# Optimization experiments

Hardware: AMD Instinct MI355X
Metric: run time of the kernel (lower is better)

Reference implementation:

```python
import jax, jax.numpy as jnp
import numpy as np

B, N, M, D = 8, 4096, 4096, 3


def setup_inputs() -> dict:
    key = jax.random.key(0)
    k1, k2 = jax.random.split(key)
    preds = jax.random.normal(k1, (B, M, D), dtype=jnp.float32)
    gts = jax.random.normal(k2, (B, N, D), dtype=jnp.float32)
    c = jnp.ones((1,), dtype=jnp.float32)
    return {"preds": preds, "gts": gts, "c": c}


def _huber(x, c):
    return jnp.where(x < c, 0.5 * x * x, c * x - 0.5 * c * c)


def reference(preds, gts, c):
    # P[b, i, j] = ||gts[b,i] - preds[b,j]||^2  (as in batch_pairwise_dist(gts, preds))
    rx = jnp.sum(gts * gts, axis=-1)              # [B, N]
    ry = jnp.sum(preds * preds, axis=-1)          # [B, M]
    zz = jnp.einsum('bnd,bmd->bnm', gts, preds)   # [B, N, M]
    P = rx[:, :, None] + ry[:, None, :] - 2.0 * zz
    mins1 = jnp.min(P, axis=1)                    # [B, M] min over gts
    mins2 = jnp.min(P, axis=2)                    # [B, N] min over preds
    loss = jnp.sum(_huber(mins1, c)) + jnp.sum(_huber(mins2, c))
    return loss
```

## Files before the change

### kernel.cpp

```cpp
#include <hip/hip_runtime.h>

typedef float v2f __attribute__((ext_vector_type(2)));
typedef float v4f __attribute__((ext_vector_type(4)));

#define NPTS   4096
#define CHUNK  256
#define G4     (CHUNK / 4)
#define QPT    4
#define TPB    256
#define QPB    (TPB * QPT)
#define NCHUNK (NPTS / CHUNK)
#define NZ     16

__device__ __forceinline__ v2f pk_fma(v2f a, v2f b, v2f c) {
    v2f d;
    asm("v_pk_fma_f32 %0, %1, %2, %3" : "=v"(d) : "v"(a), "v"(b), "v"(c));
    return d;
}
__device__ __forceinline__ float min3f(float a, float b, float c) {
    float d;
    asm("v_min3_f32 %0, %1, %2, %3" : "=v"(d) : "v"(a), "v"(b), "v"(c));
    return d;
}

__global__ __launch_bounds__(TPB, 4) void min_kernel(const float* __restrict__ preds,
                                                     const float* __restrict__ gts,
                                                     float* __restrict__ partial) {
    const int z    = blockIdx.z;
    const int b    = z >> 1;
    const int pass = z & 1;
    const float* pts = pass ? preds : gts;
    const float* qrs = pass ? gts   : preds;

    const int chunk = blockIdx.y;
    const int i0    = chunk * CHUNK;
    const int tid   = threadIdx.x;

    __shared__ v4f SX[G4], SY[G4], SZ[G4], SW[G4];

    {
        const float* pb = pts + ((size_t)b * NPTS + i0) * 3;
        float x  = pb[tid * 3 + 0];
        float y  = pb[tid * 3 + 1];
        float zz = pb[tid * 3 + 2];
        float w  = fmaf(x, x, fmaf(y, y, zz * zz));
        ((float*)SX)[tid] = x;
        ((float*)SY)[tid] = y;
        ((float*)SZ)[tid] = zz;
        ((float*)SW)[tid] = w;
    }

    const float* qb    = qrs + (size_t)b * NPTS * 3;
    const int    jbase = blockIdx.x * QPB + tid;
    v2f   AX[QPT], AY[QPT], AZ[QPT];
    float R[QPT], acc[QPT];
#pragma unroll
    for (int q = 0; q < QPT; ++q) {
        int   j  = jbase + q * TPB;
        float qx = qb[j * 3 + 0];
        float qy = qb[j * 3 + 1];
        float qz = qb[j * 3 + 2];
        R[q]   = fmaf(qx, qx, fmaf(qy, qy, qz * qz));
        float ax = -2.0f * qx, ay = -2.0f * qy, az = -2.0f * qz;
        AX[q] = (v2f){ax, ax};
        AY[q] = (v2f){ay, ay};
        AZ[q] = (v2f){az, az};
        acc[q] = 3.4e38f;
    }
    __syncthreads();

#pragma unroll 4
    for (int g = 0; g < G4; ++g) {
        v4f X = SX[g], Y = SY[g], Z = SZ[g], W = SW[g];
        v2f xlo = X.lo, xhi = X.hi;
        v2f ylo = Y.lo, yhi = Y.hi;
        v2f zlo = Z.lo, zhi = Z.hi;
        v2f wlo = W.lo, whi = W.hi;
#pragma unroll
        for (int q = 0; q < QPT; ++q) {
            v2f t0 = pk_fma(xlo, AX[q], pk_fma(ylo, AY[q], pk_fma(zlo, AZ[q], wlo)));
            v2f t1 = pk_fma(xhi, AX[q], pk_fma(yhi, AY[q], pk_fma(zhi, AZ[q], whi)));
            acc[q] = min3f(t0.x, t0.y, min3f(t1.x, t1.y, acc[q]));
        }
    }

    float* dst = partial + ((size_t)z * NCHUNK + chunk) * NPTS;
#pragma unroll
    for (int q = 0; q < QPT; ++q) {
        dst[jbase + q * TPB] = R[q] + acc[q];
    }
}

__global__ __launch_bounds__(256) void huber_kernel(const float* __restrict__ partial,
                                                    const float* __restrict__ cp,
                                                    float* __restrict__ bp) {
    const int s = blockIdx.x * 256 + threadIdx.x;
    const int z = s >> 12, j = s & (NPTS - 1);
    const float* p = partial + (size_t)z * NCHUNK * NPTS + j;
    float m = 3.4e38f;
#pragma unroll
    for (int c = 0; c < NCHUNK; ++c) m = fminf(m, p[(size_t)c * NPTS]);
    const float cc = cp[0];
    float h = (m < cc) ? (0.5f * m * m) : fmaf(cc, m, -0.5f * cc * cc);
    for (int off = 32; off > 0; off >>= 1) h += __shfl_down(h, off, 64);
    __shared__ float ls[4];
    if ((threadIdx.x & 63) == 0) ls[threadIdx.x >> 6] = h;
    __syncthreads();
    if (threadIdx.x == 0) bp[blockIdx.x] = ls[0] + ls[1] + ls[2] + ls[3];
}

__global__ __launch_bounds__(256) void final_kernel(const float* __restrict__ bp,
                                                    float* __restrict__ out) {
    float a = bp[threadIdx.x];
    for (int off = 32; off > 0; off >>= 1) a += __shfl_down(a, off, 64);
    __shared__ float ls[4];
    if ((threadIdx.x & 63) == 0) ls[threadIdx.x >> 6] = a;
    __syncthreads();
    if (threadIdx.x == 0) out[0] = ls[0] + ls[1] + ls[2] + ls[3];
}

extern "C" void kernel_launch(void* const* d_in, const int* in_sizes, int n_in,
                              void* d_out, int out_size, void* d_ws, size_t ws_size,
                              hipStream_t stream) {
    const float* preds = (const float*)d_in[0];
    const float* gts   = (const float*)d_in[1];
    const float* cp    = (const float*)d_in[2];
    float* out = (float*)d_out;

    float* partial = (float*)d_ws;
    float* bp      = partial + (size_t)NZ * NCHUNK * NPTS;

    dim3 gm(NPTS / QPB, NCHUNK, NZ);
    min_kernel<<<gm, TPB, 0, stream>>>(preds, gts, partial);

    huber_kernel<<<(NZ * NPTS) / 256, 256, 0, stream>>>(partial, cp, bp);
    final_kernel<<<1, 256, 0, stream>>>(bp, out);
}
```

Before: 32.99 us.

## Pretranspose points to SoA, reduce mins with atomicMin, fuse huber and final

```diff
diff --git a/kernel.cpp b/kernel.cpp
--- a/kernel.cpp
+++ b/kernel.cpp
@@ -1,16 +1,27 @@
 #include <hip/hip_runtime.h>
 
-typedef float v2f __attribute__((ext_vector_type(2)));
-typedef float v4f __attribute__((ext_vector_type(4)));
+typedef float v2f  __attribute__((ext_vector_type(2)));
+typedef float v4f  __attribute__((ext_vector_type(4)));
 
 #define NPTS   4096
-#define CHUNK  256
-#define G4     (CHUNK / 4)
-#define QPT    4
+#define NB     8
+#define NZ     16
+#define QPT    8
 #define TPB    256
 #define QPB    (TPB * QPT)
-#define NCHUNK (NPTS / CHUNK)
-#define NZ     16
+#define XB     (NPTS / QPB)
+#define RANGE  128
+#define NGRP   (RANGE / 4)
+#define NRANGE (NPTS / RANGE)
+
+__device__ __forceinline__ unsigned enc_f(float f) {
+    unsigned u = __float_as_uint(f);
+    return (u & 0x80000000u) ? ~u : (u | 0x80000000u);
+}
+__device__ __forceinline__ float dec_f(unsigned e) {
+    unsigned u = (e & 0x80000000u) ? (e ^ 0x80000000u) : ~e;
+    return __uint_as_float(u);
+}
 
 __device__ __forceinline__ v2f pk_fma(v2f a, v2f b, v2f c) {
     v2f d;
@@ -23,35 +34,45 @@
     return d;
 }
 
-__global__ __launch_bounds__(TPB, 4) void min_kernel(const float* __restrict__ preds,
+__global__ __launch_bounds__(256) void prep_kernel(const float* __restrict__ preds,
+                                                   const float* __restrict__ gts,
+                                                   float* __restrict__ ptsT,
+                                                   unsigned* __restrict__ mins) {
+    const int t = blockIdx.x * 256 + threadIdx.x;
+    mins[t] = 0xFFFFFFFFu;
+    if (t < 2 * NB * (NPTS / 4)) {
+        const int arr = t >> 13;
+        const float* src = (arr ? preds : gts) + (size_t)(t & 8191) * 12;
+        v4f f0 = *(const v4f*)(src + 0);
+        v4f f1 = *(const v4f*)(src + 4);
+        v4f f2 = *(const v4f*)(src + 8);
+        float x0=f0.x, y0=f0.y, z0=f0.z, x1=f0.w;
+        float y1=f1.x, z1=f1.y, x2=f1.z, y2=f1.w;
+        float z2=f2.x, x3=f2.y, y3=f2.z, z3=f2.w;
+        v4f X = {x0, x1, x2, x3};
+        v4f Y = {y0, y1, y2, y3};
+        v4f Z = {z0, z1, z2, z3};
+        v4f W = {fmaf(x0,x0,fmaf(y0,y0,z0*z0)), fmaf(x1,x1,fmaf(y1,y1,z1*z1)),
+                 fmaf(x2,x2,fmaf(y2,y2,z2*z2)), fmaf(x3,x3,fmaf(y3,y3,z3*z3))};
+        v4f* dst = (v4f*)(ptsT + (size_t)t * 16);
+        dst[0] = X; dst[1] = Y; dst[2] = Z; dst[3] = W;
+    }
+}
+
+__global__ __launch_bounds__(TPB, 2) void min_kernel(const float* __restrict__ preds,
                                                      const float* __restrict__ gts,
-                                                     float* __restrict__ partial) {
+                                                     const float* __restrict__ ptsT,
+                                                     unsigned* __restrict__ mins) {
     const int z    = blockIdx.z;
     const int b    = z >> 1;
     const int pass = z & 1;
-    const float* pts = pass ? preds : gts;
-    const float* qrs = pass ? gts   : preds;
+    const int tid  = threadIdx.x;
 
-    const int chunk = blockIdx.y;
-    const int i0    = chunk * CHUNK;
-    const int tid   = threadIdx.x;
+    const v4f* gp = (const v4f*)ptsT
+                  + ((size_t)(pass * NB + b) * (NPTS / 4) + blockIdx.y * NGRP) * 4;
+    const float* qb = (pass ? gts : preds) + (size_t)b * NPTS * 3;
 
-    __shared__ v4f SX[G4], SY[G4], SZ[G4], SW[G4];
-
-    {
-        const float* pb = pts + ((size_t)b * NPTS + i0) * 3;
-        float x  = pb[tid * 3 + 0];
-        float y  = pb[tid * 3 + 1];
-        float zz = pb[tid * 3 + 2];
-        float w  = fmaf(x, x, fmaf(y, y, zz * zz));
-        ((float*)SX)[tid] = x;
-        ((float*)SY)[tid] = y;
-        ((float*)SZ)[tid] = zz;
-        ((float*)SW)[tid] = w;
-    }
-
-    const float* qb    = qrs + (size_t)b * NPTS * 3;
-    const int    jbase = blockIdx.x * QPB + tid;
+    const int jbase = blockIdx.x * QPB + tid;
     v2f   AX[QPT], AY[QPT], AZ[QPT];
     float R[QPT], acc[QPT];
 #pragma unroll
@@ -60,63 +81,59 @@
         float qx = qb[j * 3 + 0];
         float qy = qb[j * 3 + 1];
         float qz = qb[j * 3 + 2];
-        R[q]   = fmaf(qx, qx, fmaf(qy, qy, qz * qz));
+        R[q]  = fmaf(qx, qx, fmaf(qy, qy, qz * qz));
         float ax = -2.0f * qx, ay = -2.0f * qy, az = -2.0f * qz;
         AX[q] = (v2f){ax, ax};
         AY[q] = (v2f){ay, ay};
         AZ[q] = (v2f){az, az};
         acc[q] = 3.4e38f;
     }
-    __syncthreads();
 
 #pragma unroll 4
-    for (int g = 0; g < G4; ++g) {
-        v4f X = SX[g], Y = SY[g], Z = SZ[g], W = SW[g];
-        v2f xlo = X.lo, xhi = X.hi;
-        v2f ylo = Y.lo, yhi = Y.hi;
-        v2f zlo = Z.lo, zhi = Z.hi;
-        v2f wlo = W.lo, whi = W.hi;
+    for (int g = 0; g < NGRP; ++g) {
+        v4f X = gp[g * 4 + 0];
+        v4f Y = gp[g * 4 + 1];
+        v4f Z = gp[g * 4 + 2];
+        v4f W = gp[g * 4 + 3];
+        v2f Xlo = X.lo, Xhi = X.hi;
+        v2f Ylo = Y.lo, Yhi = Y.hi;
+        v2f Zlo = Z.lo, Zhi = Z.hi;
+        v2f Wlo = W.lo, Whi = W.hi;
 #pragma unroll
         for (int q = 0; q < QPT; ++q) {
-            v2f t0 = pk_fma(xlo, AX[q], pk_fma(ylo, AY[q], pk_fma(zlo, AZ[q], wlo)));
-            v2f t1 = pk_fma(xhi, AX[q], pk_fma(yhi, AY[q], pk_fma(zhi, AZ[q], whi)));
+            v2f t0 = pk_fma(Xlo, AX[q], pk_fma(Ylo, AY[q], pk_fma(Zlo, AZ[q], Wlo)));
+            v2f t1 = pk_fma(Xhi, AX[q], pk_fma(Yhi, AY[q], pk_fma(Zhi, AZ[q], Whi)));
             acc[q] = min3f(t0.x, t0.y, min3f(t1.x, t1.y, acc[q]));
         }
     }
 
-    float* dst = partial + ((size_t)z * NCHUNK + chunk) * NPTS;
+    unsigned* mz = mins + (size_t)z * NPTS;
 #pragma unroll
     for (int q = 0; q < QPT; ++q) {
-        dst[jbase + q * TPB] = R[q] + acc[q];
+        atomicMin(&mz[jbase + q * TPB], enc_f(R[q] + acc[q]));
     }
 }
 
-__global__ __launch_bounds__(256) void huber_kernel(const float* __restrict__ partial,
-                                                    const float* __restrict__ cp,
-                                                    float* __restrict__ bp) {
-    const int s = blockIdx.x * 256 + threadIdx.x;
-    const int z = s >> 12, j = s & (NPTS - 1);
-    const float* p = partial + (size_t)z * NCHUNK * NPTS + j;
-    float m = 3.4e38f;
+__global__ __launch_bounds__(1024) void huberfinal_kernel(const unsigned* __restrict__ mins,
+                                                          const float* __restrict__ cp,
+                                                          float* __restrict__ out) {
+    const float c = cp[0];
+    float acc = 0.0f;
+#pragma unroll 4
+    for (int i = threadIdx.x; i < NZ * NPTS; i += 1024) {
+        float x = dec_f(mins[i]);
+        acc += (x < c) ? (0.5f * x * x) : fmaf(c, x, -0.5f * c * c);
+    }
+    for (int off = 32; off > 0; off >>= 1) acc += __shfl_down(acc, off, 64);
+    __shared__ float ls[16];
+    if ((threadIdx.x & 63) == 0) ls[threadIdx.x >> 6] = acc;
+    __syncthreads();
+    if (threadIdx.x == 0) {
+        float s = 0.0f;
 #pragma unroll
-    for (int c = 0; c < NCHUNK; ++c) m = fminf(m, p[(size_t)c * NPTS]);
-    const float cc = cp[0];
-    float h = (m < cc) ? (0.5f * m * m) : fmaf(cc, m, -0.5f * cc * cc);
-    for (int off = 32; off > 0; off >>= 1) h += __shfl_down(h, off, 64);
-    __shared__ float ls[4];
-    if ((threadIdx.x & 63) == 0) ls[threadIdx.x >> 6] = h;
-    __syncthreads();
-    if (threadIdx.x == 0) bp[blockIdx.x] = ls[0] + ls[1] + ls[2] + ls[3];
-}
-
-__global__ __launch_bounds__(256) void final_kernel(const float* __restrict__ bp,
-                                                    float* __restrict__ out) {
-    float a = bp[threadIdx.x];
-    for (int off = 32; off > 0; off >>= 1) a += __shfl_down(a, off, 64);
-    __shared__ float ls[4];
-    if ((threadIdx.x & 63) == 0) ls[threadIdx.x >> 6] = a;
-    __syncthreads();
-    if (threadIdx.x == 0) out[0] = ls[0] + ls[1] + ls[2] + ls[3];
+        for (int w = 0; w < 16; ++w) s += ls[w];
+        out[0] = s;
+    }
 }
 
 extern "C" void kernel_launch(void* const* d_in, const int* in_sizes, int n_in,
@@ -127,12 +144,13 @@
     const float* cp    = (const float*)d_in[2];
     float* out = (float*)d_out;
 
-    float* partial = (float*)d_ws;
-    float* bp      = partial + (size_t)NZ * NCHUNK * NPTS;
+    float*    ptsT = (float*)d_ws;
+    unsigned* mins = (unsigned*)(ptsT + (size_t)2 * NB * (NPTS / 4) * 16);
 
-    dim3 gm(NPTS / QPB, NCHUNK, NZ);
-    min_kernel<<<gm, TPB, 0, stream>>>(preds, gts, partial);
+    prep_kernel<<<(NZ * NPTS) / 256, 256, 0, stream>>>(preds, gts, ptsT, mins);
 
-    huber_kernel<<<(NZ * NPTS) / 256, 256, 0, stream>>>(partial, cp, bp);
-    final_kernel<<<1, 256, 0, stream>>>(bp, out);
+    dim3 gm(XB, NRANGE, NZ);
+    min_kernel<<<gm, TPB, 0, stream>>>(preds, gts, ptsT, mins);
+
+    huberfinal_kernel<<<1, 1024, 0, stream>>>(mins, cp, out);
 }
```

Result: slower. 42.07 us (+27.5%).
